# Kernel optimization log

Measured on AMD Instinct MI355X. Metric: run time of the kernel, lower is better.

## Reference

```python
import jax, jax.numpy as jnp
import numpy as np

D_MODEL = 1024
NHEAD = 16
DHEAD = D_MODEL // NHEAD
DFF = 4096
B, S = 2, 2048
R = 25                # local_attention_radius = 5*5
K = 5                 # rel_pos_max_distance
W = 2 * R + 1         # window width
EPS = 1e-5


def setup_inputs() -> dict:
    key = jax.random.key(0)
    ks = jax.random.split(key, 12)
    s = 0.02
    g = lambda k, shape: jax.random.normal(k, shape, jnp.float32) * s
    return {
        "src": jax.random.normal(ks[0], (B, S, D_MODEL), jnp.float32),
        # attention in/out projections (W stored [out,in], applied x @ W.T + b)
        "wq": g(ks[1], (D_MODEL, D_MODEL)), "bq": jnp.zeros((D_MODEL,), jnp.float32),
        "wk": g(ks[2], (D_MODEL, D_MODEL)), "bk": jnp.zeros((D_MODEL,), jnp.float32),
        "wv": g(ks[3], (D_MODEL, D_MODEL)), "bv": jnp.zeros((D_MODEL,), jnp.float32),
        "wo": g(ks[4], (D_MODEL, D_MODEL)), "bo": jnp.zeros((D_MODEL,), jnp.float32),
        # relative position embeddings, ids clipped to [-K, K] -> 2K+1 rows
        "rel_emb": g(ks[5], (2 * K + 1, DHEAD)),
        # FFN
        "w1": g(ks[6], (DFF, D_MODEL)), "b1": jnp.zeros((DFF,), jnp.float32),
        "w2": g(ks[7], (D_MODEL, DFF)), "b2": jnp.zeros((D_MODEL,), jnp.float32),
        # layernorms
        "g1": jnp.ones((D_MODEL,), jnp.float32), "beta1": jnp.zeros((D_MODEL,), jnp.float32),
        "g2": jnp.ones((D_MODEL,), jnp.float32), "beta2": jnp.zeros((D_MODEL,), jnp.float32),
    }


def _layernorm(x, g, b):
    m = x.mean(-1, keepdims=True)
    v = ((x - m) ** 2).mean(-1, keepdims=True)
    return (x - m) * jax.lax.rsqrt(v + EPS) * g + b


def _rel_window_attention(x, wq, bq, wk, bk, wv, bv, wo, bo, rel_emb):
    b, s, d = x.shape

    def proj(w, bias):
        return (x @ w.T + bias).reshape(b, s, NHEAD, DHEAD).transpose(0, 2, 1, 3)

    q = proj(wq, bq)  # [B,H,S,Dh]
    k = proj(wk, bk)
    v = proj(wv, bv)

    offsets = jnp.arange(-R, R + 1)                     # [W]
    j = jnp.arange(s)[:, None] + offsets[None, :]       # [S,W] absolute key index
    valid = (j >= 0) & (j < s)
    jc = jnp.clip(j, 0, s - 1)

    scale = 1.0 / np.sqrt(DHEAD).astype(np.float32)
    k_win = k[:, :, jc]                                 # [B,H,S,W,Dh] banded gather
    scores = jnp.einsum('bhsd,bhswd->bhsw', q, k_win) * scale
    rel_ids = jnp.clip(offsets, -K, K) + K              # [W]
    scores = scores + jnp.einsum('bhsd,wd->bhsw', q, rel_emb[rel_ids]) * scale
    scores = jnp.where(valid[None, None], scores, jnp.float32(-1e30))
    attn = jax.nn.softmax(scores, axis=-1)              # [B,H,S,W]

    v_win = v[:, :, jc]                                 # [B,H,S,W,Dh]
    out = jnp.einsum('bhsw,bhswd->bhsd', attn, v_win)
    out = out.transpose(0, 2, 1, 3).reshape(b, s, d)
    return out @ wo.T + bo


def reference(src, wq, bq, wk, bk, wv, bv, wo, bo, rel_emb,
              w1, b1, w2, b2, g1, beta1, g2, beta2):
    # post-norm (norm_first=False default) transformer block, dropout=0 (eval)
    z = _rel_window_attention(src, wq, bq, wk, bk, wv, bv, wo, bo, rel_emb)
    x = _layernorm(src + z, g1, beta1)
    ff = jax.nn.relu(x @ w1.T + b1) @ w2.T + b2
    return _layernorm(x + ff, g2, beta2)
```

## Files before the change

### kernel.cpp

```cpp
#include <hip/hip_runtime.h>


#define D_MODEL 1024
#define SEQ     2048
#define NROWS   4096
#define WIN     51
#define RAD     25

typedef __attribute__((ext_vector_type(8))) __bf16 bf16x8;
typedef __attribute__((ext_vector_type(4))) float  floatx4;

__device__ __forceinline__ unsigned short f2bf(float x) {
    unsigned u = __float_as_uint(x);
    unsigned r = u + 0x7fffu + ((u >> 16) & 1u);
    return (unsigned short)(r >> 16);
}
__device__ __forceinline__ float bf2f(unsigned short h) {
    return __uint_as_float(((unsigned)h) << 16);
}

__device__ __forceinline__ void gld16(const unsigned short* g, unsigned short* l) {
    __builtin_amdgcn_global_load_lds(
        (const __attribute__((address_space(1))) unsigned int*)g,
        (__attribute__((address_space(3))) unsigned int*)l,
        16, 0, 0);
}

__device__ __forceinline__ void cvtgrp(const float* __restrict__ in,
                                       unsigned short* __restrict__ out, int g) {
    float4 f = ((const float4*)in)[g];
    ushort4 u;
    u.x = f2bf(f.x); u.y = f2bf(f.y); u.z = f2bf(f.z); u.w = f2bf(f.w);
    ((ushort4*)out)[g] = u;
}

__global__ __launch_bounds__(256)
void cvt_all(const float* __restrict__ src,
             const float* __restrict__ wq, const float* __restrict__ wk,
             const float* __restrict__ wv, const float* __restrict__ wo,
             const float* __restrict__ w1, const float* __restrict__ w2,
             const float* __restrict__ bq, const float* __restrict__ bk,
             const float* __restrict__ bv,
             unsigned short* __restrict__ xb,
             unsigned short* __restrict__ wqkvb,
             unsigned short* __restrict__ wob,
             unsigned short* __restrict__ w1b,
             unsigned short* __restrict__ w2b,
             float* __restrict__ bqkv)
{
    int g = blockIdx.x * 256 + threadIdx.x;
    if (g >= 4194496) return;
    if (g < 1048576) { cvtgrp(src, xb, g); return; }
    g -= 1048576;
    if (g < 262144) { cvtgrp(wq, wqkvb, g); return; }
    g -= 262144;
    if (g < 262144) { cvtgrp(wk, wqkvb + 1048576, g); return; }
    g -= 262144;
    if (g < 262144) { cvtgrp(wv, wqkvb + 2097152, g); return; }
    g -= 262144;
    if (g < 262144) { cvtgrp(wo, wob, g); return; }
    g -= 262144;
    if (g < 1048576) { cvtgrp(w1, w1b, g); return; }
    g -= 1048576;
    if (g < 1048576) { cvtgrp(w2, w2b, g); return; }
    g -= 1048576;
    float4 f = (g < 64) ? ((const float4*)bq)[g]
             : (g < 128) ? ((const float4*)bk)[g - 64]
                         : ((const float4*)bv)[g - 128];
    ((float4*)bqkv)[g] = f;
}

#define BM 128
#define BN 128
#define BK 32

__global__ __launch_bounds__(256, 4)
void gemm_bt(const unsigned short* __restrict__ A,
             const unsigned short* __restrict__ Wt,
             const float* __restrict__ bias,
             unsigned short* __restrict__ Cb,
             int kstride, int kloop, int T, int ldc, int relu)
{
    __shared__ __attribute__((aligned(16))) unsigned short As[2][BM * BK];
    __shared__ __attribute__((aligned(16))) unsigned short Bs[2][BN * BK];

    const int id = blockIdx.x;
    const int s  = id / T;
    const int t  = id - s * T;
    const int sid  = (t & 7) * (T >> 3) + (t >> 3);
    const int rect = sid >> 5;
    const int r    = sid & 31;
    const int bm = ((rect & 7) * 4 + (r >> 3)) * BM;
    const int bn = ((rect >> 3) * 8 + (r & 7)) * BN;

    const int tid  = threadIdx.x;
    const int lane = tid & 63;
    const int wave = tid >> 6;
    const int wm = (wave >> 1) * 64;
    const int wn = (wave & 1) * 64;

    const int srow = lane >> 2;
    const int scol = ((lane & 3) ^ ((lane >> 3) & 3)) * 8;
    const int kofs = s * kloop;
    const unsigned short* Ag = A  + (size_t)(bm + wave * 32 + srow) * kstride + kofs + scol;
    const unsigned short* Wg = Wt + (size_t)(bn + wave * 32 + srow) * kstride + kofs + scol;
    const size_t tstep = (size_t)16 * kstride;
    const int lb = wave * 1024;

    const int fm  = lane & 15;
    const int pg8 = ((lane >> 4) ^ ((fm >> 1) & 3)) * 8;

    floatx4 acc[4][4] = {};
    const int iters = kloop >> 5;

    auto issue = [&](int j, int b) {
        const unsigned short* Aj = Ag + j * BK;
        const unsigned short* Wj = Wg + j * BK;
        gld16(Aj,         &As[b][lb]);
        gld16(Aj + tstep, &As[b][lb + 512]);
        gld16(Wj,         &Bs[b][lb]);
        gld16(Wj + tstep, &Bs[b][lb + 512]);
    };

    issue(0, 0);

    for (int j = 0; j < iters; j++) {
        const int cur = j & 1;
        __syncthreads();
        if (j + 1 < iters) issue(j + 1, cur ^ 1);

        bf16x8 af[4], bf[4];
        #pragma unroll
        for (int ii = 0; ii < 4; ii++)
            af[ii] = *(const bf16x8*)(&As[cur][(wm + ii * 16 + fm) * BK + pg8]);
        #pragma unroll
        for (int jj = 0; jj < 4; jj++)
            bf[jj] = *(const bf16x8*)(&Bs[cur][(wn + jj * 16 + fm) * BK + pg8]);
        #pragma unroll
        for (int ii = 0; ii < 4; ii++)
            #pragma unroll
            for (int jj = 0; jj < 4; jj++)
                acc[ii][jj] = __builtin_amdgcn_mfma_f32_16x16x32_bf16(
                    af[ii], bf[jj], acc[ii][jj], 0, 0, 0);
    }

    unsigned short* Co = Cb + (size_t)s * NROWS * ldc;
    const int r0 = bm + wm + (lane >> 4) * 4;
    const int c0e = bn + wn + (lane & 15);
    #pragma unroll
    for (int i = 0; i < 4; i++) {
        #pragma unroll
        for (int j = 0; j < 4; j++) {
            const int col = c0e + j * 16;
            const float bv = bias ? bias[col] : 0.0f;
            #pragma unroll
            for (int rr = 0; rr < 4; rr++) {
                const int row = r0 + i * 16 + rr;
                float v = acc[i][j][rr] + bv;
                if (relu) v = fmaxf(v, 0.0f);
                Co[(size_t)row * ldc + col] = f2bf(v);
            }
        }
    }
}

__global__ __launch_bounds__(256, 2)
void attn_mfma(const unsigned short* __restrict__ qkv,
               const float* __restrict__ rel,
               unsigned short* __restrict__ attnb)
{
    __shared__ __attribute__((aligned(16))) unsigned short Qs[64 * 72];
    __shared__ __attribute__((aligned(16))) unsigned short Ks[128 * 72];
    __shared__ __attribute__((aligned(16))) unsigned short Vt[64 * 168];
    __shared__ __attribute__((aligned(16))) unsigned short Rs[16 * 72];
    __shared__ __attribute__((aligned(16))) unsigned short Pl[4 * 16 * 104];
    __shared__ float Qrl[4 * 16 * 12];

    const int t   = threadIdx.x;
    const int blk = blockIdx.x;
    const int st  = blk & 31;
    const int h   = (blk >> 5) & 15;
    const int b   = blk >> 9;
    const int s0  = st << 6;
    const int brow0 = b * SEQ;

    const int trow = t >> 3;
    const int tc   = (t & 7) * 8;
    const uint4 z4 = make_uint4(0, 0, 0, 0);

    #pragma unroll
    for (int p = 0; p < 2; p++) {
        int r = trow + p * 32;
        uint4 v = *(const uint4*)(qkv + (size_t)(brow0 + s0 + r) * 3072 + h * 64 + tc);
        *(uint4*)(Qs + r * 72 + tc) = v;
    }
    #pragma unroll
    for (int p = 0; p < 4; p++) {
        int kr = trow + p * 32;
        int ka = s0 - 25 + kr;
        bool in = (ka >= 0) & (ka < SEQ);
        uint4 kv = z4, vv = z4;
        if (in) {
            kv = *(const uint4*)(qkv + (size_t)(brow0 + ka) * 3072 + 1024 + h * 64 + tc);
            vv = *(const uint4*)(qkv + (size_t)(brow0 + ka) * 3072 + 2048 + h * 64 + tc);
        }
        *(uint4*)(Ks + kr * 72 + tc) = kv;
        const unsigned short* e = (const unsigned short*)&vv;
        #pragma unroll
        for (int j = 0; j < 8; j++)
            Vt[(tc + j) * 168 + kr] = e[j];
    }
    if (t < 176) {
        float4 f = ((const float4*)rel)[t];
        int fi = t * 4, rr = fi >> 6, cc = fi & 63;
        ushort4 u;
        u.x = f2bf(f.x); u.y = f2bf(f.y); u.z = f2bf(f.z); u.w = f2bf(f.w);
        *(ushort4*)(Rs + rr * 72 + cc) = u;
    } else {
        int fi = 704 + (t - 176) * 4, rr = fi >> 6, cc = fi & 63;
        *(ushort4*)(Rs + rr * 72 + cc) = make_ushort4(0, 0, 0, 0);
    }
    {
        int n = t * 4, w2 = n >> 8, rem = n & 255, rr = rem >> 4, cc = 80 + (rem & 15);
        *(ushort4*)(Pl + w2 * (16 * 104) + rr * 104 + cc) = make_ushort4(0, 0, 0, 0);
    }
    for (int idx = t; idx < 320; idx += 256) {
        int r = idx / 5, cchunk = idx % 5;
        *(uint4*)(Vt + r * 168 + 128 + cchunk * 8) = z4;
    }
    __syncthreads();

    const int wave = t >> 6;
    const int lane = t & 63;
    const int fm   = lane & 15;
    const int fk8  = (lane >> 4) * 8;
    const int S0w  = s0 + wave * 16;
    unsigned short* Plw = Pl + wave * (16 * 104);
    float* Ql = Qrl + wave * (16 * 12);

    bf16x8 qa0 = *(const bf16x8*)(Qs + (wave * 16 + fm) * 72 + fk8);
    bf16x8 qa1 = *(const bf16x8*)(Qs + (wave * 16 + fm) * 72 + fk8 + 32);

    floatx4 Sc[5];
    #pragma unroll
    for (int nt = 0; nt < 5; nt++) {
        bf16x8 kb0 = *(const bf16x8*)(Ks + (wave * 16 + nt * 16 + fm) * 72 + fk8);
        bf16x8 kb1 = *(const bf16x8*)(Ks + (wave * 16 + nt * 16 + fm) * 72 + fk8 + 32);
        floatx4 acc = {0.f, 0.f, 0.f, 0.f};
        acc = __builtin_amdgcn_mfma_f32_16x16x32_bf16(qa0, kb0, acc, 0, 0, 0);
        acc = __builtin_amdgcn_mfma_f32_16x16x32_bf16(qa1, kb1, acc, 0, 0, 0);
        Sc[nt] = acc;
    }
    {
        bf16x8 rb0 = *(const bf16x8*)(Rs + fm * 72 + fk8);
        bf16x8 rb1 = *(const bf16x8*)(Rs + fm * 72 + fk8 + 32);
        floatx4 qr = {0.f, 0.f, 0.f, 0.f};
        qr = __builtin_amdgcn_mfma_f32_16x16x32_bf16(qa0, rb0, qr, 0, 0, 0);
        qr = __builtin_amdgcn_mfma_f32_16x16x32_bf16(qa1, rb1, qr, 0, 0, 0);
        if (fm < 12) {
            #pragma unroll
            for (int reg = 0; reg < 4; reg++)
                Ql[((lane >> 4) * 4 + reg) * 12 + fm] = qr[reg];
        }
    }

    float inv[4];
    const int iq0 = (lane >> 4) * 4;
    #pragma unroll
    for (int reg = 0; reg < 4; reg++) {
        const int i = iq0 + reg;
        float sc[5];
        float mx = -1e30f;
        #pragma unroll
        for (int nt = 0; nt < 5; nt++) {
            int c   = nt * 16 + fm;
            int off = c - 25 - i;
            int ka  = S0w - 25 + c;
            bool valid = (off >= -RAD) & (off <= RAD) & (ka >= 0) & (ka < SEQ);
            int rid = min(max(off, -5), 5) + 5;
            float v = valid ? (Sc[nt][reg] + Ql[i * 12 + rid]) * 0.125f : -1e30f;
            sc[nt] = v;
            mx = fmaxf(mx, v);
        }
        #pragma unroll
        for (int o = 1; o < 16; o <<= 1) mx = fmaxf(mx, __shfl_xor(mx, o));
        float sum = 0.f;
        #pragma unroll
        for (int nt = 0; nt < 5; nt++) {
            float e = __expf(sc[nt] - mx);
            sum += e;
            Plw[i * 104 + nt * 16 + fm] = f2bf(e);
        }
        #pragma unroll
        for (int o = 1; o < 16; o <<= 1) sum += __shfl_xor(sum, o);
        inv[reg] = 1.0f / sum;
    }

    floatx4 O[4] = {};
    #pragma unroll
    for (int kc = 0; kc < 3; kc++) {
        bf16x8 pa = *(const bf16x8*)(Plw + fm * 104 + fk8 + kc * 32);
        #pragma unroll
        for (int nt = 0; nt < 4; nt++) {
            bf16x8 vb = *(const bf16x8*)(Vt + (nt * 16 + fm) * 168 + wave * 16 + fk8 + kc * 32);
            O[nt] = __builtin_amdgcn_mfma_f32_16x16x32_bf16(pa, vb, O[nt], 0, 0, 0);
        }
    }

    #pragma unroll
    for (int nt = 0; nt < 4; nt++) {
        const int d = nt * 16 + fm;
        #pragma unroll
        for (int reg = 0; reg < 4; reg++) {
            const int i = iq0 + reg;
            attnb[(size_t)(brow0 + S0w + i) * 1024 + h * 64 + d] = f2bf(O[nt][reg] * inv[reg]);
        }
    }
}

__global__ __launch_bounds__(256)
void ln_fuse(const float* __restrict__ resf,
             const unsigned short* __restrict__ resb,
             const unsigned short* __restrict__ p0,
             const unsigned short* __restrict__ p1,
             const float* __restrict__ cbias,
             const float* __restrict__ gamma,
             const float* __restrict__ beta,
             float* __restrict__ outf,
             unsigned short* __restrict__ outb)
{
    const int wave = threadIdx.x >> 6;
    const int lane = threadIdx.x & 63;
    const int row = blockIdx.x * 4 + wave;
    const size_t base = (size_t)row * D_MODEL;

    float x[16];
    float sum = 0.0f, sq = 0.0f;
    #pragma unroll
    for (int i = 0; i < 4; i++) {
        const int c4 = lane + i * 64;
        ushort4 u0 = ((const ushort4*)(p0 + base))[c4];
        ushort4 u1 = ((const ushort4*)(p1 + base))[c4];
        float4 cb = ((const float4*)cbias)[c4];
        float4 va;
        if (resf) {
            va = ((const float4*)(resf + base))[c4];
        } else {
            ushort4 ua = ((const ushort4*)(resb + base))[c4];
            va.x = bf2f(ua.x); va.y = bf2f(ua.y); va.z = bf2f(ua.z); va.w = bf2f(ua.w);
        }
        float e0 = va.x + bf2f(u0.x) + bf2f(u1.x) + cb.x;
        float e1 = va.y + bf2f(u0.y) + bf2f(u1.y) + cb.y;
        float e2 = va.z + bf2f(u0.z) + bf2f(u1.z) + cb.z;
        float e3 = va.w + bf2f(u0.w) + bf2f(u1.w) + cb.w;
        x[i*4+0] = e0; x[i*4+1] = e1; x[i*4+2] = e2; x[i*4+3] = e3;
        sum += e0 + e1 + e2 + e3;
        sq  += e0*e0 + e1*e1 + e2*e2 + e3*e3;
    }
    #pragma unroll
    for (int off = 32; off > 0; off >>= 1) {
        sum += __shfl_xor(sum, off);
        sq  += __shfl_xor(sq,  off);
    }
    const float mean = sum * (1.0f / 1024.0f);
    const float var  = sq  * (1.0f / 1024.0f) - mean * mean;
    const float rs   = rsqrtf(var + 1e-5f);

    #pragma unroll
    for (int i = 0; i < 4; i++) {
        const int c4 = lane + i * 64;
        float4 g4 = ((const float4*)gamma)[c4];
        float4 b4 = ((const float4*)beta)[c4];
        float4 o;
        o.x = (x[i*4+0] - mean) * rs * g4.x + b4.x;
        o.y = (x[i*4+1] - mean) * rs * g4.y + b4.y;
        o.z = (x[i*4+2] - mean) * rs * g4.z + b4.z;
        o.w = (x[i*4+3] - mean) * rs * g4.w + b4.w;
        if (outf) ((float4*)(outf + base))[c4] = o;
        if (outb) {
            ushort4 u;
            u.x = f2bf(o.x); u.y = f2bf(o.y); u.z = f2bf(o.z); u.w = f2bf(o.w);
            ((ushort4*)(outb + base))[c4] = u;
        }
    }
}

extern "C" void kernel_launch(void* const* d_in, const int* in_sizes, int n_in,
                              void* d_out, int out_size, void* d_ws, size_t ws_size,
                              hipStream_t stream)
{
    const float* src = (const float*)d_in[0];
    const float* wq  = (const float*)d_in[1];
    const float* bq  = (const float*)d_in[2];
    const float* wk  = (const float*)d_in[3];
    const float* bk  = (const float*)d_in[4];
    const float* wv  = (const float*)d_in[5];
    const float* bv  = (const float*)d_in[6];
    const float* wo  = (const float*)d_in[7];
    const float* bo  = (const float*)d_in[8];
    const float* rel = (const float*)d_in[9];
    const float* w1  = (const float*)d_in[10];
    const float* b1  = (const float*)d_in[11];
    const float* w2  = (const float*)d_in[12];
    const float* b2  = (const float*)d_in[13];
    const float* g1  = (const float*)d_in[14];
    const float* be1 = (const float*)d_in[15];
    const float* g2  = (const float*)d_in[16];
    const float* be2 = (const float*)d_in[17];
    float* out = (float*)d_out;

    char* ws = (char*)d_ws;
    const size_t MB = 1048576;
    unsigned short* wqkvb = (unsigned short*)(ws + 0);
    unsigned short* wob   = (unsigned short*)(ws + 6  * MB);
    unsigned short* w1b   = (unsigned short*)(ws + 8  * MB);
    unsigned short* w2b   = (unsigned short*)(ws + 16 * MB);
    float*          bqkv  = (float*)         (ws + 24 * MB);
    unsigned short* xb    = (unsigned short*)(ws + 25 * MB);
    unsigned short* attnb = (unsigned short*)(ws + 25 * MB);
    unsigned short* qkvb  = (unsigned short*)(ws + 33 * MB);
    unsigned short* z01   = (unsigned short*)(ws + 33 * MB);
    unsigned short* ff1b  = (unsigned short*)(ws + 33 * MB);
    unsigned short* f01   = (unsigned short*)(ws + 65 * MB);
    unsigned short* x1b   = (unsigned short*)(ws + 81 * MB);
    const size_t SL = (size_t)NROWS * 1024;

    const dim3 blk(256);
    cvt_all<<<16385, blk, 0, stream>>>(src, wq, wk, wv, wo, w1, w2, bq, bk, bv,
                                       xb, wqkvb, wob, w1b, w2b, bqkv);
    gemm_bt<<<768, blk, 0, stream>>>(xb, wqkvb, bqkv, qkvb, 1024, 1024, 768, 3072, 0);
    attn_mfma<<<1024, blk, 0, stream>>>(qkvb, rel, attnb);
    gemm_bt<<<512, blk, 0, stream>>>(attnb, wob, nullptr, z01, 1024, 512, 256, 1024, 0);
    ln_fuse<<<NROWS / 4, blk, 0, stream>>>(src, nullptr, z01, z01 + SL, bo, g1, be1,
                                           nullptr, x1b);
    gemm_bt<<<1024, blk, 0, stream>>>(x1b, w1b, b1, ff1b, 1024, 1024, 1024, 4096, 1);
    gemm_bt<<<512, blk, 0, stream>>>(ff1b, w2b, nullptr, f01, 4096, 2048, 256, 1024, 0);
    ln_fuse<<<NROWS / 4, blk, 0, stream>>>(nullptr, x1b, f01, f01 + SL, b2, g2, be2,
                                           out, nullptr);
}
```

Baseline: 309.5 us.

## Add 256x256-tile GEMM kernel with 3-stage LDS pipeline for QKV and FFN

Adds a 512-thread GEMM kernel with 256x256 output tiles, a triple-buffered direct-to-LDS load pipeline, XOR-swizzled LDS layout, setprio around MFMA bursts and a grouped tile order. It replaces the 128x128 GEMM for the QKV and both FFN projections. The FFN2 projection becomes a 4-way split-K whose partials are summed in an extended layernorm kernel, and the workspace layout is reshuffled to fit those partials. The aim is higher arithmetic intensity and better overlap of loads with MFMA, at the cost of fewer blocks (192 to 256), possible under-occupancy of the CUs, and extra partial-sum traffic.

```diff
diff --git a/kernel.cpp b/kernel.cpp
--- a/kernel.cpp
+++ b/kernel.cpp
@@ -164,6 +164,124 @@
     }
 }
 
+#define ROT3(x) ((x) == 16384 ? 0 : (x) + 8192)
+
+__global__ __launch_bounds__(512, 2)
+void gemm256(const unsigned short* __restrict__ A,
+             const unsigned short* __restrict__ Wt,
+             const float* __restrict__ bias,
+             unsigned short* __restrict__ Cb,
+             int kstride, int kloop, int T, int tncnt,
+             int ldc, int relu, size_t sstep1, size_t sstep2)
+{
+    __shared__ __attribute__((aligned(16))) unsigned short AS[3 * 8192];
+    __shared__ __attribute__((aligned(16))) unsigned short BS[3 * 8192];
+
+    const int id = blockIdx.x;
+    const int s  = id / T;
+    const int t0 = id - s * T;
+    const int sid = (t0 & 7) * (T >> 3) + (t0 >> 3);
+    const int bm = (sid / tncnt) * 256;
+    const int bn = (sid % tncnt) * 256;
+
+    const int tid  = threadIdx.x;
+    const int lane = tid & 63;
+    const int wave = tid >> 6;
+    const int wr   = wave >> 2;
+    const int wc   = wave & 3;
+    const int fm   = lane & 15;
+    const int fq   = lane >> 4;
+
+    const int kofs = s * kloop;
+    const int NT   = kloop >> 5;
+
+    const int ks  = (tid >> 3) & 7;
+    const int gi  = tid ^ ks;
+    const int r0s = gi >> 2;
+    const int c2s = gi & 3;
+    const unsigned short* Agp = A  + (size_t)(bm + r0s) * kstride + kofs + c2s * 8;
+    const unsigned short* Wgp = Wt + (size_t)(bn + r0s) * kstride + kofs + c2s * 8;
+    const size_t istep = (size_t)128 * kstride;
+
+    const int rA  = wr * 128 + fm;
+    const int rB  = wc * 64  + fm;
+    const int c0A = ((((rA << 2) | fq) ^ (fm >> 1)) << 3);
+    const int c0B = ((((rB << 2) | fq) ^ (fm >> 1)) << 3);
+
+    gld16(Agp,              AS + tid * 8);
+    gld16(Agp + istep,      AS + tid * 8 + 4096);
+    gld16(Wgp,              BS + tid * 8);
+    gld16(Wgp + istep,      BS + tid * 8 + 4096);
+    gld16(Agp + 32,         AS + 8192 + tid * 8);
+    gld16(Agp + 32 + istep, AS + 8192 + tid * 8 + 4096);
+    gld16(Wgp + 32,         BS + 8192 + tid * 8);
+    gld16(Wgp + 32 + istep, BS + 8192 + tid * 8 + 4096);
+    asm volatile("s_waitcnt vmcnt(4)" ::: "memory");
+    __builtin_amdgcn_sched_barrier(0);
+    __builtin_amdgcn_s_barrier();
+    __builtin_amdgcn_sched_barrier(0);
+
+    floatx4 acc[8][4] = {};
+    const unsigned short* Aga = Agp + 64;
+    const unsigned short* Wga = Wgp + 64;
+    int cb = 0;
+    int pb = 16384;
+
+    for (int t = 0; t < NT; t++) {
+        const bool pf = (t + 2 < NT);
+        bf16x8 af[8];
+        #pragma unroll
+        for (int mi = 0; mi < 8; mi++)
+            af[mi] = *(const bf16x8*)(AS + cb + c0A + mi * 512);
+        #pragma unroll
+        for (int ni = 0; ni < 4; ni++) {
+            bf16x8 bfr = *(const bf16x8*)(BS + cb + c0B + ni * 512);
+            if (pf) {
+                if (ni == 0) gld16(Aga,         AS + pb + tid * 8);
+                if (ni == 1) gld16(Aga + istep, AS + pb + tid * 8 + 4096);
+                if (ni == 2) gld16(Wga,         BS + pb + tid * 8);
+                if (ni == 3) gld16(Wga + istep, BS + pb + tid * 8 + 4096);
+            }
+            __builtin_amdgcn_s_setprio(1);
+            #pragma unroll
+            for (int mi = 0; mi < 8; mi++)
+                acc[mi][ni] = __builtin_amdgcn_mfma_f32_16x16x32_bf16(
+                    af[mi], bfr, acc[mi][ni], 0, 0, 0);
+            __builtin_amdgcn_s_setprio(0);
+        }
+        if (t + 1 < NT) {
+            if (pf) asm volatile("s_waitcnt vmcnt(4)" ::: "memory");
+            else    asm volatile("s_waitcnt vmcnt(0)" ::: "memory");
+            __builtin_amdgcn_sched_barrier(0);
+            __builtin_amdgcn_s_barrier();
+            __builtin_amdgcn_sched_barrier(0);
+        }
+        cb = ROT3(cb);
+        pb = ROT3(pb);
+        Aga += 32;
+        Wga += 32;
+    }
+
+    unsigned short* Co = Cb + (size_t)(s & 1) * sstep1 + (size_t)(s >> 1) * sstep2;
+    const int r0  = bm + wr * 128 + fq * 4;
+    const int c0e = bn + wc * 64 + fm;
+    #pragma unroll
+    for (int mi = 0; mi < 8; mi++) {
+        #pragma unroll
+        for (int ni = 0; ni < 4; ni++) {
+            const int col = c0e + ni * 16;
+            const float bv = bias ? bias[col] : 0.0f;
+            #pragma unroll
+            for (int rr = 0; rr < 4; rr++) {
+                const int row = r0 + mi * 16 + rr;
+                float v = acc[mi][ni][rr] + bv;
+                if (relu) v = fmaxf(v, 0.0f);
+                Co[(size_t)row * ldc + col] = f2bf(v);
+            }
+        }
+    }
+}
+
 __global__ __launch_bounds__(256, 2)
 void attn_mfma(const unsigned short* __restrict__ qkv,
                const float* __restrict__ rel,
@@ -323,6 +441,8 @@
              const unsigned short* __restrict__ resb,
              const unsigned short* __restrict__ p0,
              const unsigned short* __restrict__ p1,
+             const unsigned short* __restrict__ p2,
+             const unsigned short* __restrict__ p3,
              const float* __restrict__ cbias,
              const float* __restrict__ gamma,
              const float* __restrict__ beta,
@@ -353,6 +473,14 @@
         float e1 = va.y + bf2f(u0.y) + bf2f(u1.y) + cb.y;
         float e2 = va.z + bf2f(u0.z) + bf2f(u1.z) + cb.z;
         float e3 = va.w + bf2f(u0.w) + bf2f(u1.w) + cb.w;
+        if (p2) {
+            ushort4 u2 = ((const ushort4*)(p2 + base))[c4];
+            ushort4 u3 = ((const ushort4*)(p3 + base))[c4];
+            e0 += bf2f(u2.x) + bf2f(u3.x);
+            e1 += bf2f(u2.y) + bf2f(u3.y);
+            e2 += bf2f(u2.z) + bf2f(u3.z);
+            e3 += bf2f(u2.w) + bf2f(u3.w);
+        }
         x[i*4+0] = e0; x[i*4+1] = e1; x[i*4+2] = e2; x[i*4+3] = e3;
         sum += e0 + e1 + e2 + e3;
         sq  += e0*e0 + e1*e1 + e2*e2 + e3*e3;
@@ -417,24 +545,30 @@
     unsigned short* w2b   = (unsigned short*)(ws + 16 * MB);
     float*          bqkv  = (float*)         (ws + 24 * MB);
     unsigned short* xb    = (unsigned short*)(ws + 25 * MB);
-    unsigned short* attnb = (unsigned short*)(ws + 25 * MB);
+    unsigned short* attnb = xb;
     unsigned short* qkvb  = (unsigned short*)(ws + 33 * MB);
     unsigned short* z01   = (unsigned short*)(ws + 33 * MB);
-    unsigned short* ff1b  = (unsigned short*)(ws + 33 * MB);
-    unsigned short* f01   = (unsigned short*)(ws + 65 * MB);
-    unsigned short* x1b   = (unsigned short*)(ws + 81 * MB);
-    const size_t SL = (size_t)NROWS * 1024;
+    unsigned short* x1b   = (unsigned short*)(ws + 49 * MB);
+    unsigned short* ff1b  = (unsigned short*)(ws + 57 * MB);
+    unsigned short* f01   = (unsigned short*)(ws + 0);
+    const size_t SL    = (size_t)NROWS * 1024;
+    const size_t SOFF2 = (size_t)12 * MB;
 
     const dim3 blk(256);
+    const dim3 blk5(512);
     cvt_all<<<16385, blk, 0, stream>>>(src, wq, wk, wv, wo, w1, w2, bq, bk, bv,
                                        xb, wqkvb, wob, w1b, w2b, bqkv);
-    gemm_bt<<<768, blk, 0, stream>>>(xb, wqkvb, bqkv, qkvb, 1024, 1024, 768, 3072, 0);
+    gemm256<<<192, blk5, 0, stream>>>(xb, wqkvb, bqkv, qkvb, 1024, 1024, 192, 12,
+                                      3072, 0, 0, 0);
     attn_mfma<<<1024, blk, 0, stream>>>(qkvb, rel, attnb);
     gemm_bt<<<512, blk, 0, stream>>>(attnb, wob, nullptr, z01, 1024, 512, 256, 1024, 0);
-    ln_fuse<<<NROWS / 4, blk, 0, stream>>>(src, nullptr, z01, z01 + SL, bo, g1, be1,
-                                           nullptr, x1b);
-    gemm_bt<<<1024, blk, 0, stream>>>(x1b, w1b, b1, ff1b, 1024, 1024, 1024, 4096, 1);
-    gemm_bt<<<512, blk, 0, stream>>>(ff1b, w2b, nullptr, f01, 4096, 2048, 256, 1024, 0);
-    ln_fuse<<<NROWS / 4, blk, 0, stream>>>(nullptr, x1b, f01, f01 + SL, b2, g2, be2,
-                                           out, nullptr);
-}
+    ln_fuse<<<NROWS / 4, blk, 0, stream>>>(src, nullptr, z01, z01 + SL, nullptr, nullptr,
+                                           bo, g1, be1, nullptr, x1b);
+    gemm256<<<256, blk5, 0, stream>>>(x1b, w1b, b1, ff1b, 1024, 1024, 256, 16,
+                                      4096, 1, 0, 0);
+    gemm256<<<256, blk5, 0, stream>>>(ff1b, w2b, nullptr, f01, 4096, 1024, 64, 4,
+                                      1024, 0, SL, SOFF2);
+    ln_fuse<<<NROWS / 4, blk, 0, stream>>>(nullptr, x1b, f01, f01 + SL,
+                                           f01 + SOFF2, f01 + SOFF2 + SL,
+                                           b2, g2, be2, out, nullptr);
+}
```

After: 312.6 us. About the same (+1.0%).
